# Kernel tuning notes

Hardware: AMD Instinct MI355X
Metric: run time of the kernel (lower is better)

## Reference

```python
import jax, jax.numpy as jnp
import numpy as np

B, S, D, H = 2, 2048, 1024, 16
DH = D // H  # 64


def setup_inputs() -> dict:
    key = jax.random.key(0)
    ks = jax.random.split(key, 12)
    inp = {
        "hidden_states": jax.random.normal(ks[0], (B, S, D), dtype=jnp.float32),
        "attention_mask": jax.random.randint(ks[1], (B, S), 0, 2, dtype=jnp.int32),
        "Wq": jax.random.normal(ks[2], (D, D), dtype=jnp.float32) / np.sqrt(D),
        "bq": jnp.zeros((D,), dtype=jnp.float32),
        "Wk": jax.random.normal(ks[3], (D, D), dtype=jnp.float32) / np.sqrt(D),
        "bk": jnp.zeros((D,), dtype=jnp.float32),
        "Wv": jax.random.normal(ks[4], (D, D), dtype=jnp.float32) / np.sqrt(D),
        "bv": jnp.zeros((D,), dtype=jnp.float32),
        # per-head additive query bias (emotion manipulation path)
        "emotion_w": jax.random.normal(ks[5], (H, DH), dtype=jnp.float32),
        "Wo": jax.random.normal(ks[6], (D, D), dtype=jnp.float32) / np.sqrt(D),
        "bo": jnp.zeros((D,), dtype=jnp.float32),
    }
    return inp


def reference(hidden_states, attention_mask, Wq, bq, Wk, bk, Wv, bv, emotion_w, Wo, bo):
    b, s, d = hidden_states.shape
    # projections -> [b, h, s, dh]
    def proj(W, bias):
        y = hidden_states @ W + bias
        return y.reshape(b, s, H, DH).transpose(0, 2, 1, 3)

    q = proj(Wq, bq)
    k = proj(Wk, bk)
    v = proj(Wv, bv)

    # manipulation_type='emotion': additive per-head query bias
    q = q + emotion_w[None, :, None, :]

    scores = jnp.einsum("bhqd,bhkd->bhqk", q, k) / np.sqrt(DH).astype(np.float32)
    # key-padding mask: positions where mask==0 get -inf
    scores = jnp.where(attention_mask[:, None, None, :] == 0, -jnp.inf, scores)
    attn = jax.nn.softmax(scores, axis=-1)  # dropout is identity in eval mode

    out = jnp.einsum("bhqk,bhkd->bhqd", attn, v)
    out = out.transpose(0, 2, 1, 3).reshape(b, s, d)
    return out @ Wo + bo
```

## Files before the change

kernel.cpp:

```cpp
#include <hip/hip_runtime.h>
#include <hip/hip_bf16.h>


#define B_  2
#define S_  2048
#define D_  1024
#define K_  1024
#define H_  16
#define DH_ 64
#define BS_ (B_*S_)

typedef __hip_bfloat16 bf16;
typedef __attribute__((ext_vector_type(8))) short s8v;
typedef __attribute__((ext_vector_type(4))) short s4v;
typedef __attribute__((ext_vector_type(4))) float f4v;

__device__ __forceinline__ float b2f(bf16 x) { return __bfloat162float(x); }
__device__ __forceinline__ bf16  f2b(float x) { return __float2bfloat16(x); }

__device__ __forceinline__ void gl_lds_16B(const bf16* g, bf16* l) {
    __builtin_amdgcn_global_load_lds(
        (const __attribute__((address_space(1))) unsigned int*)g,
        (__attribute__((address_space(3))) unsigned int*)l, 16, 0, 0);
}

#define QSCALE_ 0.1803368801f

__global__ __launch_bounds__(256) void prep_kernel(
    const float* __restrict__ X, const int* __restrict__ mask,
    const float* __restrict__ Wq, const float* __restrict__ Wk,
    const float* __restrict__ Wv, const float* __restrict__ Wo,
    bf16* __restrict__ Xb, bf16* __restrict__ mkbf,
    bf16* __restrict__ WTq, bf16* __restrict__ WTk,
    bf16* __restrict__ WTv, bf16* __restrict__ WTo)
{
    __shared__ float Ls[64][68];
    const int blk = blockIdx.x;
    const int t   = threadIdx.x;

    if (blk < 1024) {
        const int z   = blk >> 8;
        const int t16 = blk & 255;
        const int k0  = (t16 >> 4) * 64;
        const int n0  = (t16 & 15) * 64;
        const float* __restrict__ W = (z == 0) ? Wq : (z == 1) ? Wk : (z == 2) ? Wv : Wo;
        bf16* __restrict__ WT       = (z == 0) ? WTq : (z == 1) ? WTk : (z == 2) ? WTv : WTo;

        const int lr = t >> 4;
        const int lc = (t & 15) * 4;
        #pragma unroll
        for (int i = 0; i < 4; i++) {
            const int k = i * 16 + lr;
            const float4 v = *(const float4*)(W + (size_t)(k0 + k) * K_ + n0 + lc);
            Ls[k][lc + 0] = v.x; Ls[k][lc + 1] = v.y;
            Ls[k][lc + 2] = v.z; Ls[k][lc + 3] = v.w;
        }
        __syncthreads();
        #pragma unroll
        for (int i = 0; i < 4; i++) {
            const int n = i * 16 + lr;
            s4v o;
            #pragma unroll
            for (int j = 0; j < 4; j++) {
                bf16 tb = f2b(Ls[lc + j][n]);
                o[j] = *(short*)&tb;
            }
            *(s4v*)(WT + (size_t)(n0 + n) * K_ + k0 + lc) = o;
        }
    } else if (blk < 5120) {
        const size_t idx = ((size_t)(blk - 1024) * 256 + t) * 4;
        const float4 v = *(const float4*)(X + idx);
        bf16 t0 = f2b(v.x), t1 = f2b(v.y), t2 = f2b(v.z), t3 = f2b(v.w);
        s4v o;
        o[0] = *(short*)&t0; o[1] = *(short*)&t1;
        o[2] = *(short*)&t2; o[3] = *(short*)&t3;
        *(s4v*)(Xb + idx) = o;
    } else {
        const int idx = (blk - 5120) * 256 + t;
        mkbf[idx] = f2b(mask[idx] ? 1.0f : 0.0f);
    }
}

template <bool SWAPPED>
__device__ __forceinline__ void gemm_tile(
    const bf16* __restrict__ A, const bf16* __restrict__ BT,
    int m0, int n0, bf16* As, bf16* Bs, f4v acc[4][4])
{
    const int t    = threadIdx.x;
    const int lane = t & 63;
    const int wave = t >> 6;
    const int quad = lane >> 4;
    const int l15  = lane & 15;
    const int wr   = wave >> 1;
    const int wc   = wave & 1;

    const int sr = t >> 3;
    const int sc = (t & 7) * 8;

    for (int kb = 0; kb < K_; kb += 64) {
        #pragma unroll
        for (int i = 0; i < 4; i++) {
            const int r = i * 32 + sr;
            gl_lds_16B(A  + (size_t)(m0 + r) * K_ + kb + sc, As + r * 64 + sc);
            gl_lds_16B(BT + (size_t)(n0 + r) * K_ + kb + sc, Bs + r * 64 + sc);
        }
        __syncthreads();

        #pragma unroll
        for (int ks = 0; ks < 2; ks++) {
            s8v fA[4], fB[4];
            #pragma unroll
            for (int i = 0; i < 4; i++) {
                fA[i] = *(const s8v*)&As[(wr * 64 + i * 16 + l15) * 64 + ks * 32 + quad * 8];
                fB[i] = *(const s8v*)&Bs[(wc * 64 + i * 16 + l15) * 64 + ks * 32 + quad * 8];
            }
            #pragma unroll
            for (int i = 0; i < 4; i++)
                #pragma unroll
                for (int j = 0; j < 4; j++)
                    acc[i][j] = SWAPPED
                        ? __builtin_amdgcn_mfma_f32_16x16x32_bf16(fB[i], fA[j], acc[i][j], 0, 0, 0)
                        : __builtin_amdgcn_mfma_f32_16x16x32_bf16(fA[i], fB[j], acc[i][j], 0, 0, 0);
        }
        __syncthreads();
    }
}

__global__ __launch_bounds__(256) void proj_qkv_kernel(
    const bf16* __restrict__ Xb,
    const bf16* __restrict__ WTq, const float* __restrict__ bq,
    const bf16* __restrict__ WTk, const float* __restrict__ bk,
    const bf16* __restrict__ WTv, const float* __restrict__ bv,
    const float* __restrict__ emo, const int* __restrict__ mask,
    bf16* __restrict__ q_ws, bf16* __restrict__ k_ws, bf16* __restrict__ v_ws)
{
    const int m0 = blockIdx.x * 128;
    const int n0 = blockIdx.y * 128;
    const int z  = blockIdx.z;

    __shared__ __align__(16) bf16 As[128 * 64];
    __shared__ __align__(16) bf16 Bs[128 * 64];

    const int t    = threadIdx.x;
    const int lane = t & 63;
    const int wave = t >> 6;
    const int quad = lane >> 4;
    const int l15  = lane & 15;
    const int wr   = wave >> 1;
    const int wc   = wave & 1;

    f4v acc[4][4] = {};

    if (z == 0) {
        gemm_tile<false>(Xb, WTq, m0, n0, As, Bs, acc);
        #pragma unroll
        for (int j = 0; j < 4; j++) {
            const int n  = n0 + wc * 64 + j * 16 + l15;
            const int h  = n >> 6, dh = n & 63;
            const float bias_n = bq[n] + emo[n];
            #pragma unroll
            for (int i = 0; i < 4; i++) {
                #pragma unroll
                for (int r = 0; r < 4; r++) {
                    const int m = m0 + wr * 64 + i * 16 + quad * 4 + r;
                    const int b = m >> 11, s = m & 2047;
                    q_ws[(((size_t)(b * H_ + h)) * S_ + s) * DH_ + dh] =
                        f2b((acc[i][j][r] + bias_n) * QSCALE_);
                }
            }
        }
    } else if (z == 1) {
        gemm_tile<false>(Xb, WTk, m0, n0, As, Bs, acc);
        #pragma unroll
        for (int j = 0; j < 4; j++) {
            const int n  = n0 + wc * 64 + j * 16 + l15;
            const int h  = n >> 6, dh = n & 63;
            const float bias_n = bk[n];
            #pragma unroll
            for (int i = 0; i < 4; i++) {
                #pragma unroll
                for (int r = 0; r < 4; r++) {
                    const int m = m0 + wr * 64 + i * 16 + quad * 4 + r;
                    const int b = m >> 11, s = m & 2047;
                    k_ws[(((size_t)(b * H_ + h)) * S_ + s) * DH_ + dh] =
                        f2b(acc[i][j][r] + bias_n);
                }
            }
        }
    } else {
        gemm_tile<true>(Xb, WTv, m0, n0, As, Bs, acc);
        #pragma unroll
        for (int j = 0; j < 4; j++) {
            const int m = m0 + wr * 64 + j * 16 + l15;
            const int b = m >> 11, s = m & 2047;
            const float msk = mask[b * S_ + s] ? 1.0f : 0.0f;
            #pragma unroll
            for (int i = 0; i < 4; i++) {
                #pragma unroll
                for (int r = 0; r < 4; r++) {
                    const int n  = n0 + wc * 64 + i * 16 + quad * 4 + r;
                    const int h  = n >> 6, dh = n & 63;
                    v_ws[(((size_t)(b * H_ + h)) * DH_ + dh) * S_ + s] =
                        f2b((acc[i][j][r] + bv[n]) * msk);
                }
            }
        }
    }
}

__global__ __launch_bounds__(256) void proj_out_kernel(
    const bf16* __restrict__ ctx, const bf16* __restrict__ WTo,
    const float* __restrict__ bo, float* __restrict__ out)
{
    const int m0 = blockIdx.x * 128;
    const int n0 = blockIdx.y * 128;

    __shared__ __align__(16) bf16 As[128 * 64];
    __shared__ __align__(16) bf16 Bs[128 * 64];

    const int t    = threadIdx.x;
    const int lane = t & 63;
    const int wave = t >> 6;
    const int quad = lane >> 4;
    const int l15  = lane & 15;
    const int wr   = wave >> 1;
    const int wc   = wave & 1;

    f4v acc[4][4] = {};
    gemm_tile<false>(ctx, WTo, m0, n0, As, Bs, acc);

    #pragma unroll
    for (int j = 0; j < 4; j++) {
        const int n = n0 + wc * 64 + j * 16 + l15;
        const float bias_n = bo[n];
        #pragma unroll
        for (int i = 0; i < 4; i++) {
            #pragma unroll
            for (int r = 0; r < 4; r++) {
                const int m = m0 + wr * 64 + i * 16 + quad * 4 + r;
                out[(size_t)m * D_ + n] = acc[i][j][r] + bias_n;
            }
        }
    }
}

#define PP_ 88

__global__ __launch_bounds__(256) void attn_kernel(
    const bf16* __restrict__ q_ws, const bf16* __restrict__ k_ws,
    const bf16* __restrict__ v_ws, const bf16* __restrict__ mkbf,
    bf16* __restrict__ ctx)
{
    const int bh = blockIdx.x;
    const int q0 = blockIdx.y * 128;
    const int b  = bh >> 4;
    const int h  = bh & 15;

    __shared__ __align__(16) bf16 k_lds[2][64 * 64];
    __shared__ __align__(16) bf16 vt_lds[2][64 * 64];
    __shared__ __align__(16) bf16 p_lds[4][32 * PP_];

    const int t    = threadIdx.x;
    const int wave = t >> 6;
    const int lane = t & 63;
    const int quad = lane >> 4;
    const int l15  = lane & 15;
    const int lxor = l15 & 7;

    s8v qf[2][2];
    #pragma unroll
    for (int qs = 0; qs < 2; qs++)
        #pragma unroll
        for (int dt = 0; dt < 2; dt++)
            qf[qs][dt] = *(const s8v*)(q_ws +
                ((size_t)bh * S_ + q0 + wave * 32 + qs * 16 + l15) * DH_ + dt * 32 + quad * 8);

    f4v oacc[2][4] = {};
    f4v osum[2]    = {};

    int srw[2], scs[2];
    #pragma unroll
    for (int c = 0; c < 2; c++) {
        const int e = c * 2048 + t * 8;
        srw[c] = e >> 6;
        scs[c] = ((e >> 3) & 7) ^ (srw[c] & 7);
    }

    auto stage = [&](int kb0, bf16* kd, bf16* vd) {
        #pragma unroll
        for (int c = 0; c < 2; c++) {
            const int e = c * 2048 + t * 8;
            const int r = srw[c], cs = scs[c];
            gl_lds_16B(k_ws + ((size_t)bh * S_ + kb0) * DH_ + r * 64 + cs * 8,
                       kd + e);
            gl_lds_16B(v_ws + ((size_t)bh * DH_ + r) * S_ + kb0 + cs * 8,
                       vd + e);
        }
    };

    stage(0, k_lds[0], vt_lds[0]);
    __syncthreads();

    int cur = 0;
    for (int kb0 = 0; kb0 < S_; kb0 += 64) {
        if (kb0 + 64 < S_)
            stage(kb0 + 64, k_lds[cur ^ 1], vt_lds[cur ^ 1]);

        const bf16* __restrict__ kc = k_lds[cur];
        const bf16* __restrict__ vc = vt_lds[cur];

        f4v sacc[2][4] = {};
        __builtin_amdgcn_s_setprio(1);
        #pragma unroll
        for (int kt = 0; kt < 4; kt++) {
            #pragma unroll
            for (int dt = 0; dt < 2; dt++) {
                const s8v kf = *(const s8v*)&kc[(kt * 16 + l15) * 64 +
                                                ((dt * 4 + quad) ^ lxor) * 8];
                #pragma unroll
                for (int qs = 0; qs < 2; qs++)
                    sacc[qs][kt] = __builtin_amdgcn_mfma_f32_16x16x32_bf16(kf, qf[qs][dt], sacc[qs][kt], 0, 0, 0);
            }
        }
        __builtin_amdgcn_s_setprio(0);

        #pragma unroll
        for (int qs = 0; qs < 2; qs++) {
            #pragma unroll
            for (int kt = 0; kt < 4; kt++) {
                float2 e01, e23;
                e01.x = exp2f(sacc[qs][kt][0]);
                e01.y = exp2f(sacc[qs][kt][1]);
                e23.x = exp2f(sacc[qs][kt][2]);
                e23.y = exp2f(sacc[qs][kt][3]);
                union { __hip_bfloat162 hh; unsigned u; } lo, hi;
                lo.hh = __float22bfloat162_rn(e01);
                hi.hh = __float22bfloat162_rn(e23);
                *(uint2*)&p_lds[wave][(qs * 16 + l15) * PP_ + kt * 16 + quad * 4] =
                    make_uint2(lo.u, hi.u);
            }
        }

        __builtin_amdgcn_s_waitcnt(0xC07F);

        #pragma unroll
        for (int kh = 0; kh < 2; kh++) {
            s8v ap[2];
            #pragma unroll
            for (int qs = 0; qs < 2; qs++)
                ap[qs] = *(const s8v*)&p_lds[wave][(qs * 16 + l15) * PP_ + kh * 32 + quad * 8];
            const s8v mv = *(const s8v*)(mkbf + (size_t)b * S_ + kb0 + kh * 32 + quad * 8);
            __builtin_amdgcn_s_setprio(1);
            #pragma unroll
            for (int nt = 0; nt < 4; nt++) {
                const s8v vf = *(const s8v*)&vc[(nt * 16 + l15) * 64 +
                                                ((kh * 4 + quad) ^ lxor) * 8];
                #pragma unroll
                for (int qs = 0; qs < 2; qs++)
                    oacc[qs][nt] = __builtin_amdgcn_mfma_f32_16x16x32_bf16(ap[qs], vf, oacc[qs][nt], 0, 0, 0);
            }
            #pragma unroll
            for (int qs = 0; qs < 2; qs++)
                osum[qs] = __builtin_amdgcn_mfma_f32_16x16x32_bf16(ap[qs], mv, osum[qs], 0, 0, 0);
            __builtin_amdgcn_s_setprio(0);
        }

        __syncthreads();
        cur ^= 1;
    }

    #pragma unroll
    for (int qs = 0; qs < 2; qs++) {
        #pragma unroll
        for (int r = 0; r < 4; r++) {
            const float inv = 1.0f / osum[qs][r];
            const int q = q0 + wave * 32 + qs * 16 + quad * 4 + r;
            #pragma unroll
            for (int nt = 0; nt < 4; nt++)
                ctx[((size_t)b * S_ + q) * D_ + h * DH_ + nt * 16 + l15] =
                    f2b(oacc[qs][nt][r] * inv);
        }
    }
}

extern "C" void kernel_launch(void* const* d_in, const int* in_sizes, int n_in,
                              void* d_out, int out_size, void* d_ws, size_t ws_size,
                              hipStream_t stream) {
    (void)in_sizes; (void)n_in; (void)out_size; (void)ws_size;

    const float* X    = (const float*)d_in[0];
    const int*   mask = (const int*)d_in[1];
    const float* Wq   = (const float*)d_in[2];
    const float* bq   = (const float*)d_in[3];
    const float* Wk   = (const float*)d_in[4];
    const float* bk   = (const float*)d_in[5];
    const float* Wv   = (const float*)d_in[6];
    const float* bv   = (const float*)d_in[7];
    const float* emo  = (const float*)d_in[8];
    const float* Wo   = (const float*)d_in[9];
    const float* bo   = (const float*)d_in[10];
    float* out = (float*)d_out;

    bf16* q_ws = (bf16*)d_ws;
    bf16* k_ws = q_ws + (size_t)BS_ * D_;
    bf16* v_ws = k_ws + (size_t)BS_ * D_;
    bf16* ctx  = v_ws + (size_t)BS_ * D_;
    bf16* Xb   = ctx  + (size_t)BS_ * D_;
    bf16* WTq  = Xb   + (size_t)BS_ * D_;
    bf16* WTk  = WTq  + (size_t)D_ * K_;
    bf16* WTv  = WTk  + (size_t)D_ * K_;
    bf16* WTo  = WTv  + (size_t)D_ * K_;
    bf16* mkbf = WTo  + (size_t)D_ * K_;

    hipLaunchKernelGGL(prep_kernel, dim3(5136), dim3(256), 0, stream,
                       X, mask, Wq, Wk, Wv, Wo, Xb, mkbf, WTq, WTk, WTv, WTo);
    hipLaunchKernelGGL(proj_qkv_kernel, dim3(BS_ / 128, D_ / 128, 3), dim3(256), 0, stream,
                       Xb, WTq, bq, WTk, bk, WTv, bv, emo, mask, q_ws, k_ws, v_ws);
    hipLaunchKernelGGL(attn_kernel, dim3(B_ * H_, S_ / 128), dim3(256), 0, stream,
                       q_ws, k_ws, v_ws, mkbf, ctx);
    hipLaunchKernelGGL(proj_out_kernel, dim3(BS_ / 128, D_ / 128), dim3(256), 0, stream,
                       ctx, WTo, bo, out);
}
```

Baseline: 233.6 us.

## Split attention block into 8 waves of 16 query rows each

The attention kernel now launches 512 threads per block, with each of 8 waves handling 16 query rows instead of 4 waves handling 32. The K/V staging is spread over more threads, so each thread issues one 16-byte load per tile instead of two. Each wave's register footprint for accumulators and Q fragments is halved. The aim is more waves to hide latency, at the cost of less K/V fragment reuse per LDS read and more barrier participants per tile.

```diff
diff --git a/kernel.cpp b/kernel.cpp
--- a/kernel.cpp
+++ b/kernel.cpp
@@ -246,7 +246,7 @@
 
 #define PP_ 88
 
-__global__ __launch_bounds__(256) void attn_kernel(
+__global__ __launch_bounds__(512) void attn_kernel(
     const bf16* __restrict__ q_ws, const bf16* __restrict__ k_ws,
     const bf16* __restrict__ v_ws, const bf16* __restrict__ mkbf,
     bf16* __restrict__ ctx)
@@ -258,7 +258,7 @@
 
     __shared__ __align__(16) bf16 k_lds[2][64 * 64];
     __shared__ __align__(16) bf16 vt_lds[2][64 * 64];
-    __shared__ __align__(16) bf16 p_lds[4][32 * PP_];
+    __shared__ __align__(16) bf16 p_lds[8][16 * PP_];
 
     const int t    = threadIdx.x;
     const int wave = t >> 6;
@@ -267,35 +267,24 @@
     const int l15  = lane & 15;
     const int lxor = l15 & 7;
 
-    s8v qf[2][2];
+    s8v qf[2];
     #pragma unroll
-    for (int qs = 0; qs < 2; qs++)
-        #pragma unroll
-        for (int dt = 0; dt < 2; dt++)
-            qf[qs][dt] = *(const s8v*)(q_ws +
-                ((size_t)bh * S_ + q0 + wave * 32 + qs * 16 + l15) * DH_ + dt * 32 + quad * 8);
-
-    f4v oacc[2][4] = {};
-    f4v osum[2]    = {};
-
-    int srw[2], scs[2];
-    #pragma unroll
-    for (int c = 0; c < 2; c++) {
-        const int e = c * 2048 + t * 8;
-        srw[c] = e >> 6;
-        scs[c] = ((e >> 3) & 7) ^ (srw[c] & 7);
-    }
+    for (int dt = 0; dt < 2; dt++)
+        qf[dt] = *(const s8v*)(q_ws +
+            ((size_t)bh * S_ + q0 + wave * 16 + l15) * DH_ + dt * 32 + quad * 8);
+
+    f4v oacc[4] = {};
+    f4v osum   = {};
+
+    const int r_st  = t >> 3;
+    const int cs_st = (t & 7) ^ (r_st & 7);
+    const int e_st  = t * 8;
 
     auto stage = [&](int kb0, bf16* kd, bf16* vd) {
-        #pragma unroll
-        for (int c = 0; c < 2; c++) {
-            const int e = c * 2048 + t * 8;
-            const int r = srw[c], cs = scs[c];
-            gl_lds_16B(k_ws + ((size_t)bh * S_ + kb0) * DH_ + r * 64 + cs * 8,
-                       kd + e);
-            gl_lds_16B(v_ws + ((size_t)bh * DH_ + r) * S_ + kb0 + cs * 8,
-                       vd + e);
-        }
+        gl_lds_16B(k_ws + ((size_t)bh * S_ + kb0 + r_st) * DH_ + cs_st * 8,
+                   kd + e_st);
+        gl_lds_16B(v_ws + ((size_t)bh * DH_ + r_st) * S_ + kb0 + cs_st * 8,
+                   vd + e_st);
     };
 
     stage(0, k_lds[0], vt_lds[0]);
@@ -309,7 +298,7 @@
         const bf16* __restrict__ kc = k_lds[cur];
         const bf16* __restrict__ vc = vt_lds[cur];
 
-        f4v sacc[2][4] = {};
+        f4v sacc[4] = {};
         __builtin_amdgcn_s_setprio(1);
         #pragma unroll
         for (int kt = 0; kt < 4; kt++) {
@@ -317,51 +306,39 @@
             for (int dt = 0; dt < 2; dt++) {
                 const s8v kf = *(const s8v*)&kc[(kt * 16 + l15) * 64 +
                                                 ((dt * 4 + quad) ^ lxor) * 8];
-                #pragma unroll
-                for (int qs = 0; qs < 2; qs++)
-                    sacc[qs][kt] = __builtin_amdgcn_mfma_f32_16x16x32_bf16(kf, qf[qs][dt], sacc[qs][kt], 0, 0, 0);
+                sacc[kt] = __builtin_amdgcn_mfma_f32_16x16x32_bf16(kf, qf[dt], sacc[kt], 0, 0, 0);
             }
         }
         __builtin_amdgcn_s_setprio(0);
 
         #pragma unroll
-        for (int qs = 0; qs < 2; qs++) {
-            #pragma unroll
-            for (int kt = 0; kt < 4; kt++) {
-                float2 e01, e23;
-                e01.x = exp2f(sacc[qs][kt][0]);
-                e01.y = exp2f(sacc[qs][kt][1]);
-                e23.x = exp2f(sacc[qs][kt][2]);
-                e23.y = exp2f(sacc[qs][kt][3]);
-                union { __hip_bfloat162 hh; unsigned u; } lo, hi;
-                lo.hh = __float22bfloat162_rn(e01);
-                hi.hh = __float22bfloat162_rn(e23);
-                *(uint2*)&p_lds[wave][(qs * 16 + l15) * PP_ + kt * 16 + quad * 4] =
-                    make_uint2(lo.u, hi.u);
-            }
+        for (int kt = 0; kt < 4; kt++) {
+            float2 e01, e23;
+            e01.x = exp2f(sacc[kt][0]);
+            e01.y = exp2f(sacc[kt][1]);
+            e23.x = exp2f(sacc[kt][2]);
+            e23.y = exp2f(sacc[kt][3]);
+            union { __hip_bfloat162 hh; unsigned u; } lo, hi;
+            lo.hh = __float22bfloat162_rn(e01);
+            hi.hh = __float22bfloat162_rn(e23);
+            *(uint2*)&p_lds[wave][l15 * PP_ + kt * 16 + quad * 4] =
+                make_uint2(lo.u, hi.u);
         }
 
         __builtin_amdgcn_s_waitcnt(0xC07F);
 
         #pragma unroll
         for (int kh = 0; kh < 2; kh++) {
-            s8v ap[2];
-            #pragma unroll
-            for (int qs = 0; qs < 2; qs++)
-                ap[qs] = *(const s8v*)&p_lds[wave][(qs * 16 + l15) * PP_ + kh * 32 + quad * 8];
+            const s8v ap = *(const s8v*)&p_lds[wave][l15 * PP_ + kh * 32 + quad * 8];
             const s8v mv = *(const s8v*)(mkbf + (size_t)b * S_ + kb0 + kh * 32 + quad * 8);
             __builtin_amdgcn_s_setprio(1);
             #pragma unroll
             for (int nt = 0; nt < 4; nt++) {
                 const s8v vf = *(const s8v*)&vc[(nt * 16 + l15) * 64 +
                                                 ((kh * 4 + quad) ^ lxor) * 8];
-                #pragma unroll
-                for (int qs = 0; qs < 2; qs++)
-                    oacc[qs][nt] = __builtin_amdgcn_mfma_f32_16x16x32_bf16(ap[qs], vf, oacc[qs][nt], 0, 0, 0);
-            }
-            #pragma unroll
-            for (int qs = 0; qs < 2; qs++)
-                osum[qs] = __builtin_amdgcn_mfma_f32_16x16x32_bf16(ap[qs], mv, osum[qs], 0, 0, 0);
+                oacc[nt] = __builtin_amdgcn_mfma_f32_16x16x32_bf16(ap, vf, oacc[nt], 0, 0, 0);
+            }
+            osum = __builtin_amdgcn_mfma_f32_16x16x32_bf16(ap, mv, osum, 0, 0, 0);
             __builtin_amdgcn_s_setprio(0);
         }
 
@@ -370,16 +347,13 @@
     }
 
     #pragma unroll
-    for (int qs = 0; qs < 2; qs++) {
-        #pragma unroll
-        for (int r = 0; r < 4; r++) {
-            const float inv = 1.0f / osum[qs][r];
-            const int q = q0 + wave * 32 + qs * 16 + quad * 4 + r;
-            #pragma unroll
-            for (int nt = 0; nt < 4; nt++)
-                ctx[((size_t)b * S_ + q) * D_ + h * DH_ + nt * 16 + l15] =
-                    f2b(oacc[qs][nt][r] * inv);
-        }
+    for (int r = 0; r < 4; r++) {
+        const float inv = 1.0f / osum[r];
+        const int q = q0 + wave * 16 + quad * 4 + r;
+        #pragma unroll
+        for (int nt = 0; nt < 4; nt++)
+            ctx[((size_t)b * S_ + q) * D_ + h * DH_ + nt * 16 + l15] =
+                f2b(oacc[nt][r] * inv);
     }
 }
 
@@ -416,7 +390,7 @@
                        X, mask, Wq, Wk, Wv, Wo, Xb, mkbf, WTq, WTk, WTv, WTo);
     hipLaunchKernelGGL(proj_qkv_kernel, dim3(BS_ / 128, D_ / 128, 3), dim3(256), 0, stream,
                        Xb, WTq, bq, WTk, bk, WTv, bv, emo, mask, q_ws, k_ws, v_ws);
-    hipLaunchKernelGGL(attn_kernel, dim3(B_ * H_, S_ / 128), dim3(256), 0, stream,
+    hipLaunchKernelGGL(attn_kernel, dim3(B_ * H_, S_ / 128), dim3(512), 0, stream,
                        q_ws, k_ws, v_ws, mkbf, ctx);
     hipLaunchKernelGGL(proj_out_kernel, dim3(BS_ / 128, D_ / 128), dim3(256), 0, stream,
                        ctx, WTo, bo, out);
```

Result: faster. 226.5 us (-3.1%).
